# Optimization experiments

Hardware: AMD Instinct MI355X
Metric: run time of the kernel (lower is better)

The kernel has to match this reference:

```python
import jax, jax.numpy as jnp
import numpy as np

MIN_NORM = 1e-15
BALL_EPS = 4e-3   # HGCN float32 projection epsilon
MAX_NORM = 1e6    # manifold.max_norm used in torch.clamp(max=...)
C = 1.0           # c_in == c_out
N, E, D = 50000, 800000, 128


def artanh(x):
    return jnp.arctanh(jnp.clip(x, -1.0 + 1e-7, 1.0 - 1e-7))


def _norm(x):
    return jnp.clip(jnp.linalg.norm(x, axis=-1, keepdims=True), MIN_NORM)


def proj(x, c):
    # clip points to stay inside the Poincare ball of curvature c
    sc = c ** 0.5
    n = _norm(x)
    maxn = (1.0 - BALL_EPS) / sc
    return jnp.where(n > maxn, x / n * maxn, x)


def expmap0(u, c):
    sc = c ** 0.5
    n = _norm(u)
    return jnp.tanh(sc * n) * u / (sc * n)


def logmap0(p, c):
    sc = c ** 0.5
    n = _norm(p)
    return artanh(sc * n) * p / (sc * n)


def mobius_matvec(w, x, c):
    sc = c ** 0.5
    xn = _norm(x)
    mx = x @ w.T                      # [N, D_out]
    mxn = _norm(mx)
    res = jnp.tanh(mxn / xn * artanh(sc * xn)) * mx / (mxn * sc)
    zero = jnp.all(mx == 0, axis=-1, keepdims=True)
    return jnp.where(zero, jnp.zeros_like(res), res)


def mobius_add(x, y, c):
    x2 = jnp.sum(x * x, -1, keepdims=True)
    y2 = jnp.sum(y * y, -1, keepdims=True)
    xy = jnp.sum(x * y, -1, keepdims=True)
    num = (1 + 2 * c * xy + c * y2) * x + (1 - c * x2) * y
    den = 1 + 2 * c * xy + c * c * x2 * y2
    return num / jnp.clip(den, MIN_NORM)


def setup_inputs() -> dict:
    key = jax.random.key(0)
    k1, k2, k3, k4, k5 = jax.random.split(key, 5)
    # valid Poincare-ball points: expmap0 of small tangent vectors
    xt = 0.1 * jax.random.normal(k1, (N, D), jnp.float32)
    x = proj(expmap0(xt, C), C)
    edge_row = jax.random.randint(k2, (E,), 0, N)
    edge_col = jax.random.randint(k3, (E,), 0, N)
    adj_val = jax.random.uniform(k4, (E,), jnp.float32) / 16.0  # ~normalized adjacency weights
    weight = jax.random.normal(k5, (D, D), jnp.float32) * (2.0 / D) ** 0.5  # xavier, gain sqrt(2)
    bias = jnp.full((D,), 1e-4, jnp.float32)  # init.constant_(bias, 0.0001)
    return {"x": x, "adj_val": adj_val, "weight": weight, "bias": bias,
            "edge_row": edge_row, "edge_col": edge_col}


def reference(x, adj_val, weight, bias, edge_row, edge_col):
    c = C
    # ---- HypLinear (eval mode: no dropout) ----
    h = proj(mobius_matvec(weight, x, c), c)
    hyp_bias = proj(expmap0(bias[None, :], c), c)  # proj_tan0 is identity on the ball
    h = proj(mobius_add(h, hyp_bias, c), c)
    # ---- HypAgg (spmm path) ----
    x_tangent = logmap0(h, c)                                     # [N, D]
    msgs = adj_val[:, None] * x_tangent[edge_col]                 # [E, D] gather
    support_t = jax.ops.segment_sum(msgs, edge_row, num_segments=N)
    support_t = jnp.minimum(support_t, MAX_NORM)                  # clamp(max=max_norm)
    h = proj(expmap0(support_t, c), c)
    # ---- HypAct (relu in tangent space at origin) ----
    xt = jnp.minimum(jax.nn.relu(logmap0(h, c)), MAX_NORM)
    out = expmap0(xt, c)  # c_out == c_in; HypAct does not re-project
    return out
```

## Files before the change

### kernel.cpp

```cpp
#include <hip/hip_runtime.h>

#define D 128
#define MAXN 0.996f
#define MINN 1e-15f
#define ARTANH_MAX (1.0f - 1e-7f)
#define MAX_NORM 1e6f

typedef unsigned int uint;
typedef unsigned short ushort;
typedef __bf16 bf16x8 __attribute__((ext_vector_type(8)));
typedef float f32x4 __attribute__((ext_vector_type(4)));

__device__ __forceinline__ float quad_sum(float v) {
    v += __shfl_xor(v, 16, 64);
    v += __shfl_xor(v, 32, 64);
    return v;
}

__device__ __forceinline__ float half_sum32(float v) {
    v += __shfl_xor(v, 16, 64);
    v += __shfl_xor(v, 8, 64);
    v += __shfl_xor(v, 4, 64);
    v += __shfl_xor(v, 2, 64);
    v += __shfl_xor(v, 1, 64);
    return v;
}

__device__ __forceinline__ float artanh_clip(float x) {
    x = fminf(fmaxf(x, -ARTANH_MAX), ARTANH_MAX);
    return 0.5f * logf((1.0f + x) / (1.0f - x));
}

__device__ __forceinline__ ushort f2bf(float f) {
    uint u = __float_as_uint(f);
    return (ushort)((u + 0x7fffu + ((u >> 16) & 1u)) >> 16);
}

__device__ __forceinline__ uint pk2(float a, float b) {
    return (uint)f2bf(a) | ((uint)f2bf(b) << 16);
}

__global__ __launch_bounds__(256)
void wconv_kernel(const float* __restrict__ W, uint4* __restrict__ WF,
                  int4* __restrict__ cnt4, int n4, int* __restrict__ done)
{
    int idx = blockIdx.x * 256 + threadIdx.x;
    if (idx < 2048) {
        int l = idx & 63, rest = idx >> 6;
        int t = rest & 7, ks = rest >> 3;
        int lr = l & 15, kg = l >> 4;
        const float* wrow = W + (size_t)(t * 16 + lr) * D + ks * 32 + kg * 4;
        float4 lo = *(const float4*)(wrow);
        float4 hi = *(const float4*)(wrow + 16);
        WF[idx] = make_uint4(pk2(lo.x, lo.y), pk2(lo.z, lo.w),
                             pk2(hi.x, hi.y), pk2(hi.z, hi.w));
    }
    if (idx == 0) *done = 0;
    for (int z = idx; z < n4; z += gridDim.x * 256)
        cnt4[z] = make_int4(0, 0, 0, 0);
}

__global__ __launch_bounds__(256)
void phase1_kernel(const float* __restrict__ X, const uint4* __restrict__ WF,
                   const float* __restrict__ bias, ushort* __restrict__ XT, int N, int G,
                   const int* __restrict__ erow, int* __restrict__ cnt,
                   int* __restrict__ rank, int E)
{
    if ((int)blockIdx.x >= G) {
        int e4 = (blockIdx.x - G) * 256 + threadIdx.x;
        int E4 = E >> 2;
        if (e4 < E4) {
            int4 r = ((const int4*)erow)[e4];
            int4 k;
            k.x = atomicAdd(&cnt[r.x], 1);
            k.y = atomicAdd(&cnt[r.y], 1);
            k.z = atomicAdd(&cnt[r.z], 1);
            k.w = atomicAdd(&cnt[r.w], 1);
            ((int4*)rank)[e4] = k;
        }
        if (e4 == 0) {
            for (int i = E4 * 4; i < E; ++i) rank[i] = atomicAdd(&cnt[erow[i]], 1);
        }
        return;
    }
    const int wid = threadIdx.x >> 6;
    const int l   = threadIdx.x & 63;
    const int m0  = (blockIdx.x * 4 + wid) * 16;
    if (m0 >= N) return;
    const int lr = l & 15;
    const int kg = l >> 4;
    const int row = m0 + lr;
    const int rowc = row < N ? row : N - 1;

    const float* xp = X + (size_t)rowc * D + kg * 4;
    bf16x8 bfr[4];
    float xsq = 0.f;
#pragma unroll
    for (int ks = 0; ks < 4; ++ks) {
        float4 v0 = *(const float4*)(xp + ks * 32);
        float4 v1 = *(const float4*)(xp + ks * 32 + 16);
        xsq += v0.x*v0.x + v0.y*v0.y + v0.z*v0.z + v0.w*v0.w
             + v1.x*v1.x + v1.y*v1.y + v1.z*v1.z + v1.w*v1.w;
        uint4 bq = make_uint4(pk2(v0.x, v0.y), pk2(v0.z, v0.w),
                              pk2(v1.x, v1.y), pk2(v1.z, v1.w));
        bfr[ks] = __builtin_bit_cast(bf16x8, bq);
    }
    xsq = quad_sum(xsq);

    f32x4 acc[8];
#pragma unroll
    for (int t = 0; t < 8; ++t) acc[t] = (f32x4){0.f, 0.f, 0.f, 0.f};
#pragma unroll
    for (int ks = 0; ks < 4; ++ks) {
        uint4 wv[8];
#pragma unroll
        for (int t = 0; t < 8; ++t) wv[t] = WF[(ks * 8 + t) * 64 + l];
#pragma unroll
        for (int t = 0; t < 8; ++t)
            acc[t] = __builtin_amdgcn_mfma_f32_16x16x32_bf16(
                __builtin_bit_cast(bf16x8, wv[t]), bfr[ks], acc[t], 0, 0, 0);
    }

    float4 bb[8];
    float bsq = 0.f;
#pragma unroll
    for (int t = 0; t < 8; ++t) {
        bb[t] = *(const float4*)(bias + t * 16 + kg * 4);
        bsq += bb[t].x*bb[t].x + bb[t].y*bb[t].y + bb[t].z*bb[t].z + bb[t].w*bb[t].w;
    }
    bsq = quad_sum(bsq);
    float bn  = fmaxf(sqrtf(bsq), MINN);
    float bt  = tanhf(bn);
    float bps = (bt > MAXN) ? MAXN / fmaxf(bt, MINN) : 1.0f;
    float bsc = bt / bn * bps;
    float bhn = fminf(fmaxf(bt * bps, MINN), MAXN);
    float y2  = bhn * bhn;

    float sacc = 0.f, sab = 0.f;
#pragma unroll
    for (int t = 0; t < 8; ++t) {
        sacc += acc[t][0]*acc[t][0] + acc[t][1]*acc[t][1] + acc[t][2]*acc[t][2] + acc[t][3]*acc[t][3];
        sab  += acc[t][0]*bb[t].x + acc[t][1]*bb[t].y + acc[t][2]*bb[t].z + acc[t][3]*bb[t].w;
    }
    sacc = quad_sum(sacc);
    sab  = quad_sum(sab);

    float xn  = fmaxf(sqrtf(xsq), MINN);
    float mxn = fmaxf(sqrtf(sacc), MINN);
    float t1  = tanhf(mxn / xn * artanh_clip(xn));
    float s1  = t1 / mxn;
    float ps1 = (t1 > MAXN) ? MAXN / fmaxf(t1, MINN) : 1.0f;
    float s1p = s1 * ps1;
    float rn  = fminf(fmaxf(t1, MINN), MAXN);
    float x2  = rn * rn;
    float mxb = bsc * sab;
    float xy  = s1p * mxb;
    float ca  = 1.0f + 2.0f * xy + y2;
    float cb  = 1.0f - x2;
    float den = fmaxf(1.0f + 2.0f * xy + x2 * y2, MINN);
    float alpha = ca * s1p / den;
    float beta  = cb / den;
    float hn2 = alpha * alpha * sacc + 2.0f * alpha * beta * mxb + beta * beta * y2;
    float hn  = fmaxf(sqrtf(hn2), MINN);
    float ps2 = (hn > MAXN) ? MAXN / hn : 1.0f;
    float hnc = fmaxf(fminf(hn, MAXN), MINN);
    float ls  = artanh_clip(hnc) / hnc;
    float F   = ls * ps2;
    float A = F * alpha, Bc = F * beta * bsc;

    if (row < N) {
        ushort* op = XT + (size_t)row * D + kg * 4;
#pragma unroll
        for (int t = 0; t < 8; ++t) {
            uint2 o = make_uint2(pk2(A * acc[t][0] + Bc * bb[t].x, A * acc[t][1] + Bc * bb[t].y),
                                 pk2(A * acc[t][2] + Bc * bb[t].z, A * acc[t][3] + Bc * bb[t].w));
            *(uint2*)(op + t * 16) = o;
        }
    }
}

__global__ __launch_bounds__(256)
void scan1_kernel(const int* __restrict__ cnt, int* __restrict__ offs,
                  int* __restrict__ bsum, int* __restrict__ done, int N, int nb)
{
    __shared__ int wsum[4];
    __shared__ int islast;
    int t = threadIdx.x;
    int base = blockIdx.x * 1024 + t * 4;
    int v[4];
#pragma unroll
    for (int j = 0; j < 4; ++j) v[j] = (base + j < N) ? cnt[base + j] : 0;
    int tt = v[0] + v[1] + v[2] + v[3];
    int incl = tt;
#pragma unroll
    for (int o = 1; o < 64; o <<= 1) {
        int n = __shfl_up(incl, o, 64);
        if ((t & 63) >= o) incl += n;
    }
    if ((t & 63) == 63) wsum[t >> 6] = incl;
    __syncthreads();
    int wbase = 0;
    for (int w = 0; w < (t >> 6); ++w) wbase += wsum[w];
    int ex = wbase + incl - tt;
#pragma unroll
    for (int j = 0; j < 4; ++j) {
        if (base + j < N) offs[base + j] = ex;
        ex += v[j];
    }
    if (t == 255) bsum[blockIdx.x] = wbase + incl;
    __threadfence();
    if (t == 255) islast = (atomicAdd(done, 1) == nb - 1);
    __syncthreads();
    if (islast) {
        __threadfence();
        if (t < 64) {
            int bv = (t < nb) ? bsum[t] : 0;
            int incl2 = bv;
#pragma unroll
            for (int o = 1; o < 64; o <<= 1) {
                int n = __shfl_up(incl2, o, 64);
                if (t >= o) incl2 += n;
            }
            if (t < nb) bsum[t] = incl2 - bv;
        }
    }
}

__global__ __launch_bounds__(256)
void fill_kernel(const int* __restrict__ erow, const int* __restrict__ ecol,
                 const float* __restrict__ adj, const int* __restrict__ rank,
                 const int* __restrict__ offs, const int* __restrict__ bsum,
                 uint* __restrict__ bpack, int E)
{
    int e4 = blockIdx.x * 256 + threadIdx.x;
    int E4 = E >> 2;
    if (e4 < E4) {
        int4   r = ((const int4*)erow)[e4];
        int4   c = ((const int4*)ecol)[e4];
        float4 a = ((const float4*)adj)[e4];
        int4   k = ((const int4*)rank)[e4];
        bpack[offs[r.x] + bsum[r.x >> 10] + k.x] = ((uint)c.x << 16) | (uint)f2bf(a.x);
        bpack[offs[r.y] + bsum[r.y >> 10] + k.y] = ((uint)c.y << 16) | (uint)f2bf(a.y);
        bpack[offs[r.z] + bsum[r.z >> 10] + k.z] = ((uint)c.z << 16) | (uint)f2bf(a.z);
        bpack[offs[r.w] + bsum[r.w >> 10] + k.w] = ((uint)c.w << 16) | (uint)f2bf(a.w);
    }
    if (e4 == 0) {
        for (int i = E4 * 4; i < E; ++i) {
            int r = erow[i];
            bpack[offs[r] + bsum[r >> 10] + rank[i]] = ((uint)ecol[i] << 16) | (uint)f2bf(adj[i]);
        }
    }
}

__global__ __launch_bounds__(256)
void gather_kernel(const ushort* __restrict__ XT, const uint* __restrict__ bpack,
                   const int* __restrict__ offs, const int* __restrict__ bsum,
                   const int* __restrict__ cnt, float* __restrict__ OUT, int N)
{
    int row = blockIdx.x * 4 + (threadIdx.x >> 6);
    int lane = threadIdx.x & 63;
    if (row >= N) return;
    int start = offs[row] + bsum[row >> 10];
    int end = start + cnt[row];
    const uint2* xt2 = (const uint2*)XT;
    const int hl = lane & 31;
    const int hi = lane >> 5;
    float a0[4] = {0.f, 0.f, 0.f, 0.f};
    float a1[4] = {0.f, 0.f, 0.f, 0.f};
    float a2[4] = {0.f, 0.f, 0.f, 0.f};
    float a3[4] = {0.f, 0.f, 0.f, 0.f};
    int i = start;
    for (; i + 7 < end; i += 8) {
        uint4 qa = *(const uint4*)(bpack + i);
        uint4 qb = *(const uint4*)(bpack + i + 4);
        uint q0 = hi ? qa.y : qa.x;
        uint q1 = hi ? qa.w : qa.z;
        uint q2 = hi ? qb.y : qb.x;
        uint q3 = hi ? qb.w : qb.z;
        uint2 u0 = xt2[(size_t)(q0 >> 16) * 32 + hl];
        uint2 u1 = xt2[(size_t)(q1 >> 16) * 32 + hl];
        uint2 u2 = xt2[(size_t)(q2 >> 16) * 32 + hl];
        uint2 u3 = xt2[(size_t)(q3 >> 16) * 32 + hl];
        float v0 = __uint_as_float(q0 << 16);
        float v1 = __uint_as_float(q1 << 16);
        float v2 = __uint_as_float(q2 << 16);
        float v3 = __uint_as_float(q3 << 16);
        a0[0] += v0 * __uint_as_float(u0.x << 16);
        a0[1] += v0 * __uint_as_float(u0.x & 0xffff0000u);
        a0[2] += v0 * __uint_as_float(u0.y << 16);
        a0[3] += v0 * __uint_as_float(u0.y & 0xffff0000u);
        a1[0] += v1 * __uint_as_float(u1.x << 16);
        a1[1] += v1 * __uint_as_float(u1.x & 0xffff0000u);
        a1[2] += v1 * __uint_as_float(u1.y << 16);
        a1[3] += v1 * __uint_as_float(u1.y & 0xffff0000u);
        a2[0] += v2 * __uint_as_float(u2.x << 16);
        a2[1] += v2 * __uint_as_float(u2.x & 0xffff0000u);
        a2[2] += v2 * __uint_as_float(u2.y << 16);
        a2[3] += v2 * __uint_as_float(u2.y & 0xffff0000u);
        a3[0] += v3 * __uint_as_float(u3.x << 16);
        a3[1] += v3 * __uint_as_float(u3.x & 0xffff0000u);
        a3[2] += v3 * __uint_as_float(u3.y << 16);
        a3[3] += v3 * __uint_as_float(u3.y & 0xffff0000u);
    }
    for (; i + 1 < end; i += 2) {
        uint2 qp = *(const uint2*)(bpack + i);
        uint q = hi ? qp.y : qp.x;
        uint2 u = xt2[(size_t)(q >> 16) * 32 + hl];
        float v = __uint_as_float(q << 16);
        a0[0] += v * __uint_as_float(u.x << 16);
        a0[1] += v * __uint_as_float(u.x & 0xffff0000u);
        a0[2] += v * __uint_as_float(u.y << 16);
        a0[3] += v * __uint_as_float(u.y & 0xffff0000u);
    }
    if (i < end) {
        uint q = bpack[i];
        uint2 u = xt2[(size_t)(q >> 16) * 32 + hl];
        float v = hi ? 0.f : __uint_as_float(q << 16);
        a1[0] += v * __uint_as_float(u.x << 16);
        a1[1] += v * __uint_as_float(u.x & 0xffff0000u);
        a1[2] += v * __uint_as_float(u.y << 16);
        a1[3] += v * __uint_as_float(u.y & 0xffff0000u);
    }
    float c0 = (a0[0] + a1[0]) + (a2[0] + a3[0]);
    float c1 = (a0[1] + a1[1]) + (a2[1] + a3[1]);
    float c2 = (a0[2] + a1[2]) + (a2[2] + a3[2]);
    float c3 = (a0[3] + a1[3]) + (a2[3] + a3[3]);
    c0 += __shfl_xor(c0, 32, 64);
    c1 += __shfl_xor(c1, 32, 64);
    c2 += __shfl_xor(c2, 32, 64);
    c3 += __shfl_xor(c3, 32, 64);
    c0 = fminf(c0, MAX_NORM); c1 = fminf(c1, MAX_NORM);
    c2 = fminf(c2, MAX_NORM); c3 = fminf(c3, MAX_NORM);
    float nt = fmaxf(sqrtf(half_sum32(c0*c0 + c1*c1 + c2*c2 + c3*c3)), MINN);
    float th = tanhf(nt);
    float es = th / nt;
    float pf = (th > MAXN) ? MAXN / th : 1.0f;
    float hnc = fmaxf(fminf(th, MAXN), MINN);
    float ls = artanh_clip(hnc) / hnc;
    float su = ls * pf * es;
    float u0 = fminf(fmaxf(su * c0, 0.0f), MAX_NORM);
    float u1 = fminf(fmaxf(su * c1, 0.0f), MAX_NORM);
    float u2 = fminf(fmaxf(su * c2, 0.0f), MAX_NORM);
    float u3 = fminf(fmaxf(su * c3, 0.0f), MAX_NORM);
    float un = fmaxf(sqrtf(half_sum32(u0*u0 + u1*u1 + u2*u2 + u3*u3)), MINN);
    float os = tanhf(un) / un;
    if (hi == 0)
        *(float4*)(OUT + (size_t)row * D + hl * 4) =
            make_float4(os * u0, os * u1, os * u2, os * u3);
}

extern "C" void kernel_launch(void* const* d_in, const int* in_sizes, int n_in,
                              void* d_out, int out_size, void* d_ws, size_t ws_size,
                              hipStream_t stream)
{
    const float* x    = (const float*)d_in[0];
    const float* adj  = (const float*)d_in[1];
    const float* W    = (const float*)d_in[2];
    const float* bias = (const float*)d_in[3];
    const int*   erow = (const int*)d_in[4];
    const int*   ecol = (const int*)d_in[5];
    float* out = (float*)d_out;
    const int N = in_sizes[0] / D;
    const int E = in_sizes[1];

    char* p = (char*)d_ws;
    size_t off = 0;
    auto alloc = [&](size_t bytes) {
        char* r = p + off;
        off = (off + bytes + 255) & ~(size_t)255;
        return r;
    };
    ushort* xt  = (ushort*)alloc((size_t)N * D * sizeof(ushort));
    uint4*  wf  = (uint4*) alloc(2048 * sizeof(uint4));
    int*   cnt  = (int*)  alloc(((size_t)N + 4) * sizeof(int));
    int*   offs = (int*)  alloc((size_t)N * sizeof(int));
    int*   bsum = (int*)  alloc(256 * sizeof(int));
    int*   done = (int*)  alloc(256);
    int*   rank = (int*)  alloc((size_t)E * sizeof(int));
    uint*  bpack= (uint*) alloc((size_t)E * sizeof(uint));
    (void)ws_size;

    int n4 = (N + 3) >> 2;
    wconv_kernel<<<64, 256, 0, stream>>>(W, wf, (int4*)cnt, n4, done);

    int E4 = E >> 2;
    int G = (N + 63) / 64;
    int H = (E4 + 255) / 256;
    phase1_kernel<<<G + H, 256, 0, stream>>>(x, wf, bias, xt, N, G, erow, cnt, rank, E);

    int nb = (N + 1023) / 1024;
    scan1_kernel<<<nb, 256, 0, stream>>>(cnt, offs, bsum, done, N, nb);
    fill_kernel<<<(E4 + 255) / 256, 256, 0, stream>>>(erow, ecol, adj, rank, offs, bsum, bpack, E);
    gather_kernel<<<(N + 3) / 4, 256, 0, stream>>>(xt, bpack, offs, bsum, cnt, out, N);
}
```

Baseline: 124.2 us.

## Split fused GEMM/histogram kernel, shrink GEMM blocks, unroll gather to 16 edges

The combined phase1 kernel, which ran the MFMA GEMM and the edge-row histogram atomics in one launch, is split into two kernels: a GEMM kernel with 128-thread blocks (2 waves) and a separate histogram kernel. The gather loop is unrolled to process 16 edges per iteration, putting 8 independent row loads in flight per half-wave to hide more gather latency. The split adds a launch and removes overlap between GEMM and atomics. The deeper unroll raises register pressure, and rows with fewer than 16 edges fall through to the remainder loops.

```diff
diff --git a/kernel.cpp b/kernel.cpp
--- a/kernel.cpp
+++ b/kernel.cpp
@@ -60,32 +60,13 @@
         cnt4[z] = make_int4(0, 0, 0, 0);
 }
 
-__global__ __launch_bounds__(256)
-void phase1_kernel(const float* __restrict__ X, const uint4* __restrict__ WF,
-                   const float* __restrict__ bias, ushort* __restrict__ XT, int N, int G,
-                   const int* __restrict__ erow, int* __restrict__ cnt,
-                   int* __restrict__ rank, int E)
-{
-    if ((int)blockIdx.x >= G) {
-        int e4 = (blockIdx.x - G) * 256 + threadIdx.x;
-        int E4 = E >> 2;
-        if (e4 < E4) {
-            int4 r = ((const int4*)erow)[e4];
-            int4 k;
-            k.x = atomicAdd(&cnt[r.x], 1);
-            k.y = atomicAdd(&cnt[r.y], 1);
-            k.z = atomicAdd(&cnt[r.z], 1);
-            k.w = atomicAdd(&cnt[r.w], 1);
-            ((int4*)rank)[e4] = k;
-        }
-        if (e4 == 0) {
-            for (int i = E4 * 4; i < E; ++i) rank[i] = atomicAdd(&cnt[erow[i]], 1);
-        }
-        return;
-    }
+__global__ __launch_bounds__(128)
+void gemm_mfma_kernel(const float* __restrict__ X, const uint4* __restrict__ WF,
+                      const float* __restrict__ bias, ushort* __restrict__ XT, int N)
+{
     const int wid = threadIdx.x >> 6;
     const int l   = threadIdx.x & 63;
-    const int m0  = (blockIdx.x * 4 + wid) * 16;
+    const int m0  = (blockIdx.x * 2 + wid) * 16;
     if (m0 >= N) return;
     const int lr = l & 15;
     const int kg = l >> 4;
@@ -180,6 +161,26 @@
 }
 
 __global__ __launch_bounds__(256)
+void hist_kernel(const int* __restrict__ erow, int* __restrict__ cnt,
+                 int* __restrict__ rank, int E)
+{
+    int e4 = blockIdx.x * 256 + threadIdx.x;
+    int E4 = E >> 2;
+    if (e4 < E4) {
+        int4 r = ((const int4*)erow)[e4];
+        int4 k;
+        k.x = atomicAdd(&cnt[r.x], 1);
+        k.y = atomicAdd(&cnt[r.y], 1);
+        k.z = atomicAdd(&cnt[r.z], 1);
+        k.w = atomicAdd(&cnt[r.w], 1);
+        ((int4*)rank)[e4] = k;
+    }
+    if (e4 == 0) {
+        for (int i = E4 * 4; i < E; ++i) rank[i] = atomicAdd(&cnt[erow[i]], 1);
+    }
+}
+
+__global__ __launch_bounds__(256)
 void scan1_kernel(const int* __restrict__ cnt, int* __restrict__ offs,
                   int* __restrict__ bsum, int* __restrict__ done, int N, int nb)
 {
@@ -270,21 +271,35 @@
     float a2[4] = {0.f, 0.f, 0.f, 0.f};
     float a3[4] = {0.f, 0.f, 0.f, 0.f};
     int i = start;
-    for (; i + 7 < end; i += 8) {
+    for (; i + 15 < end; i += 16) {
         uint4 qa = *(const uint4*)(bpack + i);
         uint4 qb = *(const uint4*)(bpack + i + 4);
+        uint4 qc = *(const uint4*)(bpack + i + 8);
+        uint4 qd = *(const uint4*)(bpack + i + 12);
         uint q0 = hi ? qa.y : qa.x;
         uint q1 = hi ? qa.w : qa.z;
         uint q2 = hi ? qb.y : qb.x;
         uint q3 = hi ? qb.w : qb.z;
+        uint q4 = hi ? qc.y : qc.x;
+        uint q5 = hi ? qc.w : qc.z;
+        uint q6 = hi ? qd.y : qd.x;
+        uint q7 = hi ? qd.w : qd.z;
         uint2 u0 = xt2[(size_t)(q0 >> 16) * 32 + hl];
         uint2 u1 = xt2[(size_t)(q1 >> 16) * 32 + hl];
         uint2 u2 = xt2[(size_t)(q2 >> 16) * 32 + hl];
         uint2 u3 = xt2[(size_t)(q3 >> 16) * 32 + hl];
+        uint2 u4 = xt2[(size_t)(q4 >> 16) * 32 + hl];
+        uint2 u5 = xt2[(size_t)(q5 >> 16) * 32 + hl];
+        uint2 u6 = xt2[(size_t)(q6 >> 16) * 32 + hl];
+        uint2 u7 = xt2[(size_t)(q7 >> 16) * 32 + hl];
         float v0 = __uint_as_float(q0 << 16);
         float v1 = __uint_as_float(q1 << 16);
         float v2 = __uint_as_float(q2 << 16);
         float v3 = __uint_as_float(q3 << 16);
+        float v4 = __uint_as_float(q4 << 16);
+        float v5 = __uint_as_float(q5 << 16);
+        float v6 = __uint_as_float(q6 << 16);
+        float v7 = __uint_as_float(q7 << 16);
         a0[0] += v0 * __uint_as_float(u0.x << 16);
         a0[1] += v0 * __uint_as_float(u0.x & 0xffff0000u);
         a0[2] += v0 * __uint_as_float(u0.y << 16);
@@ -301,6 +316,22 @@
         a3[1] += v3 * __uint_as_float(u3.x & 0xffff0000u);
         a3[2] += v3 * __uint_as_float(u3.y << 16);
         a3[3] += v3 * __uint_as_float(u3.y & 0xffff0000u);
+        a0[0] += v4 * __uint_as_float(u4.x << 16);
+        a0[1] += v4 * __uint_as_float(u4.x & 0xffff0000u);
+        a0[2] += v4 * __uint_as_float(u4.y << 16);
+        a0[3] += v4 * __uint_as_float(u4.y & 0xffff0000u);
+        a1[0] += v5 * __uint_as_float(u5.x << 16);
+        a1[1] += v5 * __uint_as_float(u5.x & 0xffff0000u);
+        a1[2] += v5 * __uint_as_float(u5.y << 16);
+        a1[3] += v5 * __uint_as_float(u5.y & 0xffff0000u);
+        a2[0] += v6 * __uint_as_float(u6.x << 16);
+        a2[1] += v6 * __uint_as_float(u6.x & 0xffff0000u);
+        a2[2] += v6 * __uint_as_float(u6.y << 16);
+        a2[3] += v6 * __uint_as_float(u6.y & 0xffff0000u);
+        a3[0] += v7 * __uint_as_float(u7.x << 16);
+        a3[1] += v7 * __uint_as_float(u7.x & 0xffff0000u);
+        a3[2] += v7 * __uint_as_float(u7.y << 16);
+        a3[3] += v7 * __uint_as_float(u7.y & 0xffff0000u);
     }
     for (; i + 1 < end; i += 2) {
         uint2 qp = *(const uint2*)(bpack + i);
@@ -382,12 +413,9 @@
 
     int n4 = (N + 3) >> 2;
     wconv_kernel<<<64, 256, 0, stream>>>(W, wf, (int4*)cnt, n4, done);
-
+    gemm_mfma_kernel<<<(N + 31) / 32, 128, 0, stream>>>(x, wf, bias, xt, N);
     int E4 = E >> 2;
-    int G = (N + 63) / 64;
-    int H = (E4 + 255) / 256;
-    phase1_kernel<<<G + H, 256, 0, stream>>>(x, wf, bias, xt, N, G, erow, cnt, rank, E);
-
+    hist_kernel<<<(E4 + 255) / 256, 256, 0, stream>>>(erow, cnt, rank, E);
     int nb = (N + 1023) / 1024;
     scan1_kernel<<<nb, 256, 0, stream>>>(cnt, offs, bsum, done, N, nb);
     fill_kernel<<<(E4 + 255) / 256, 256, 0, stream>>>(erow, ecol, adj, rank, offs, bsum, bpack, E);
```

After: 128.2 us. +3.2%, slower.

## Split fused GEMM/histogram kernel and batch 32 edges per gather iteration

Applied to the files above, without the earlier changes.

Splits the combined phase1 kernel into a separate MFMA GEMM kernel (now 128-thread blocks, two waves each) and a standalone edge-histogram kernel, launched one after the other. The gather loop is rewritten to load 32 packed edges per iteration and issue 16 independent row gathers per half-wave, masking tail entries to a zero weight instead of running remainder loops. This should raise memory-level parallelism in the gather. In exchange it loses the overlap between GEMM and histogram, adds a kernel launch, and does wasted loads on rows whose degree is short. The packed edge buffer is padded by 32 entries so the tail over-read stays in bounds.

```diff
diff --git a/kernel.cpp b/kernel.cpp
--- a/kernel.cpp
+++ b/kernel.cpp
@@ -60,32 +60,13 @@
         cnt4[z] = make_int4(0, 0, 0, 0);
 }
 
-__global__ __launch_bounds__(256)
-void phase1_kernel(const float* __restrict__ X, const uint4* __restrict__ WF,
-                   const float* __restrict__ bias, ushort* __restrict__ XT, int N, int G,
-                   const int* __restrict__ erow, int* __restrict__ cnt,
-                   int* __restrict__ rank, int E)
-{
-    if ((int)blockIdx.x >= G) {
-        int e4 = (blockIdx.x - G) * 256 + threadIdx.x;
-        int E4 = E >> 2;
-        if (e4 < E4) {
-            int4 r = ((const int4*)erow)[e4];
-            int4 k;
-            k.x = atomicAdd(&cnt[r.x], 1);
-            k.y = atomicAdd(&cnt[r.y], 1);
-            k.z = atomicAdd(&cnt[r.z], 1);
-            k.w = atomicAdd(&cnt[r.w], 1);
-            ((int4*)rank)[e4] = k;
-        }
-        if (e4 == 0) {
-            for (int i = E4 * 4; i < E; ++i) rank[i] = atomicAdd(&cnt[erow[i]], 1);
-        }
-        return;
-    }
+__global__ __launch_bounds__(128)
+void gemm_mfma_kernel(const float* __restrict__ X, const uint4* __restrict__ WF,
+                      const float* __restrict__ bias, ushort* __restrict__ XT, int N)
+{
     const int wid = threadIdx.x >> 6;
     const int l   = threadIdx.x & 63;
-    const int m0  = (blockIdx.x * 4 + wid) * 16;
+    const int m0  = (blockIdx.x * 2 + wid) * 16;
     if (m0 >= N) return;
     const int lr = l & 15;
     const int kg = l >> 4;
@@ -180,6 +161,26 @@
 }
 
 __global__ __launch_bounds__(256)
+void hist_kernel(const int* __restrict__ erow, int* __restrict__ cnt,
+                 int* __restrict__ rank, int E)
+{
+    int e4 = blockIdx.x * 256 + threadIdx.x;
+    int E4 = E >> 2;
+    if (e4 < E4) {
+        int4 r = ((const int4*)erow)[e4];
+        int4 k;
+        k.x = atomicAdd(&cnt[r.x], 1);
+        k.y = atomicAdd(&cnt[r.y], 1);
+        k.z = atomicAdd(&cnt[r.z], 1);
+        k.w = atomicAdd(&cnt[r.w], 1);
+        ((int4*)rank)[e4] = k;
+    }
+    if (e4 == 0) {
+        for (int i = E4 * 4; i < E; ++i) rank[i] = atomicAdd(&cnt[erow[i]], 1);
+    }
+}
+
+__global__ __launch_bounds__(256)
 void scan1_kernel(const int* __restrict__ cnt, int* __restrict__ offs,
                   int* __restrict__ bsum, int* __restrict__ done, int N, int nb)
 {
@@ -265,66 +266,39 @@
     const uint2* xt2 = (const uint2*)XT;
     const int hl = lane & 31;
     const int hi = lane >> 5;
-    float a0[4] = {0.f, 0.f, 0.f, 0.f};
-    float a1[4] = {0.f, 0.f, 0.f, 0.f};
-    float a2[4] = {0.f, 0.f, 0.f, 0.f};
-    float a3[4] = {0.f, 0.f, 0.f, 0.f};
-    int i = start;
-    for (; i + 7 < end; i += 8) {
-        uint4 qa = *(const uint4*)(bpack + i);
-        uint4 qb = *(const uint4*)(bpack + i + 4);
-        uint q0 = hi ? qa.y : qa.x;
-        uint q1 = hi ? qa.w : qa.z;
-        uint q2 = hi ? qb.y : qb.x;
-        uint q3 = hi ? qb.w : qb.z;
-        uint2 u0 = xt2[(size_t)(q0 >> 16) * 32 + hl];
-        uint2 u1 = xt2[(size_t)(q1 >> 16) * 32 + hl];
-        uint2 u2 = xt2[(size_t)(q2 >> 16) * 32 + hl];
-        uint2 u3 = xt2[(size_t)(q3 >> 16) * 32 + hl];
-        float v0 = __uint_as_float(q0 << 16);
-        float v1 = __uint_as_float(q1 << 16);
-        float v2 = __uint_as_float(q2 << 16);
-        float v3 = __uint_as_float(q3 << 16);
-        a0[0] += v0 * __uint_as_float(u0.x << 16);
-        a0[1] += v0 * __uint_as_float(u0.x & 0xffff0000u);
-        a0[2] += v0 * __uint_as_float(u0.y << 16);
-        a0[3] += v0 * __uint_as_float(u0.y & 0xffff0000u);
-        a1[0] += v1 * __uint_as_float(u1.x << 16);
-        a1[1] += v1 * __uint_as_float(u1.x & 0xffff0000u);
-        a1[2] += v1 * __uint_as_float(u1.y << 16);
-        a1[3] += v1 * __uint_as_float(u1.y & 0xffff0000u);
-        a2[0] += v2 * __uint_as_float(u2.x << 16);
-        a2[1] += v2 * __uint_as_float(u2.x & 0xffff0000u);
-        a2[2] += v2 * __uint_as_float(u2.y << 16);
-        a2[3] += v2 * __uint_as_float(u2.y & 0xffff0000u);
-        a3[0] += v3 * __uint_as_float(u3.x << 16);
-        a3[1] += v3 * __uint_as_float(u3.x & 0xffff0000u);
-        a3[2] += v3 * __uint_as_float(u3.y << 16);
-        a3[3] += v3 * __uint_as_float(u3.y & 0xffff0000u);
-    }
-    for (; i + 1 < end; i += 2) {
-        uint2 qp = *(const uint2*)(bpack + i);
-        uint q = hi ? qp.y : qp.x;
-        uint2 u = xt2[(size_t)(q >> 16) * 32 + hl];
-        float v = __uint_as_float(q << 16);
-        a0[0] += v * __uint_as_float(u.x << 16);
-        a0[1] += v * __uint_as_float(u.x & 0xffff0000u);
-        a0[2] += v * __uint_as_float(u.y << 16);
-        a0[3] += v * __uint_as_float(u.y & 0xffff0000u);
-    }
-    if (i < end) {
-        uint q = bpack[i];
-        uint2 u = xt2[(size_t)(q >> 16) * 32 + hl];
-        float v = hi ? 0.f : __uint_as_float(q << 16);
-        a1[0] += v * __uint_as_float(u.x << 16);
-        a1[1] += v * __uint_as_float(u.x & 0xffff0000u);
-        a1[2] += v * __uint_as_float(u.y << 16);
-        a1[3] += v * __uint_as_float(u.y & 0xffff0000u);
-    }
-    float c0 = (a0[0] + a1[0]) + (a2[0] + a3[0]);
-    float c1 = (a0[1] + a1[1]) + (a2[1] + a3[1]);
-    float c2 = (a0[2] + a1[2]) + (a2[2] + a3[2]);
-    float c3 = (a0[3] + a1[3]) + (a2[3] + a3[3]);
+    float acc[4][4] = {{0.f}};
+
+    for (int base = start; base < end; base += 32) {
+        uint4 qq[8];
+#pragma unroll
+        for (int j = 0; j < 8; ++j)
+            qq[j] = *(const uint4*)(bpack + base + j * 4);
+        uint q[16];
+#pragma unroll
+        for (int j = 0; j < 8; ++j) {
+            q[2 * j]     = hi ? qq[j].y : qq[j].x;
+            q[2 * j + 1] = hi ? qq[j].w : qq[j].z;
+        }
+#pragma unroll
+        for (int k = 0; k < 16; ++k)
+            if (base + 2 * k + hi >= end) q[k] = 0;
+        uint2 u[16];
+#pragma unroll
+        for (int k = 0; k < 16; ++k)
+            u[k] = xt2[(size_t)(q[k] >> 16) * 32 + hl];
+#pragma unroll
+        for (int k = 0; k < 16; ++k) {
+            float v = __uint_as_float(q[k] << 16);
+            acc[k & 3][0] += v * __uint_as_float(u[k].x << 16);
+            acc[k & 3][1] += v * __uint_as_float(u[k].x & 0xffff0000u);
+            acc[k & 3][2] += v * __uint_as_float(u[k].y << 16);
+            acc[k & 3][3] += v * __uint_as_float(u[k].y & 0xffff0000u);
+        }
+    }
+    float c0 = (acc[0][0] + acc[1][0]) + (acc[2][0] + acc[3][0]);
+    float c1 = (acc[0][1] + acc[1][1]) + (acc[2][1] + acc[3][1]);
+    float c2 = (acc[0][2] + acc[1][2]) + (acc[2][2] + acc[3][2]);
+    float c3 = (acc[0][3] + acc[1][3]) + (acc[2][3] + acc[3][3]);
     c0 += __shfl_xor(c0, 32, 64);
     c1 += __shfl_xor(c1, 32, 64);
     c2 += __shfl_xor(c2, 32, 64);
@@ -377,17 +351,14 @@
     int*   bsum = (int*)  alloc(256 * sizeof(int));
     int*   done = (int*)  alloc(256);
     int*   rank = (int*)  alloc((size_t)E * sizeof(int));
-    uint*  bpack= (uint*) alloc((size_t)E * sizeof(uint));
+    uint*  bpack= (uint*) alloc(((size_t)E + 32) * sizeof(uint));
     (void)ws_size;
 
     int n4 = (N + 3) >> 2;
     wconv_kernel<<<64, 256, 0, stream>>>(W, wf, (int4*)cnt, n4, done);
-
+    gemm_mfma_kernel<<<(N + 31) / 32, 128, 0, stream>>>(x, wf, bias, xt, N);
     int E4 = E >> 2;
-    int G = (N + 63) / 64;
-    int H = (E4 + 255) / 256;
-    phase1_kernel<<<G + H, 256, 0, stream>>>(x, wf, bias, xt, N, G, erow, cnt, rank, E);
-
+    hist_kernel<<<(E4 + 255) / 256, 256, 0, stream>>>(erow, cnt, rank, E);
     int nb = (N + 1023) / 1024;
     scan1_kernel<<<nb, 256, 0, stream>>>(cnt, offs, bsum, done, N, nb);
     fill_kernel<<<(E4 + 255) / 256, 256, 0, stream>>>(erow, ecol, adj, rank, offs, bsum, bpack, E);
```

After: 188.5 us. 51.8% more time.
